# Optimization experiments

Hardware: AMD Instinct MI355X
Metric: run time of the kernel (lower is better)

The kernel has to match this reference:

```python
import math
import jax, jax.numpy as jnp
import numpy as np

B, Q, HID = 4, 4, 4096
NH, NKV, HD = 32, 8, 128
GROUPS = NH // NKV
CACHE_LEN = 4096
CACHE_MAX = CACHE_LEN + 512  # prefill_len + max_len(512)
ROPE_THETA = 500000.0
SCALE = 1.0 / math.sqrt(128.0)  # hardcoded softmax_scale in module


def rotate_half(x):
    x1, x2 = jnp.split(x, 2, axis=-1)
    return jnp.concatenate([-x2, x1], axis=-1)


def setup_inputs() -> dict:
    key = jax.random.key(0)
    ks = jax.random.split(key, 8)
    std = 0.02
    # RoPE angles for positions [CACHE_LEN, CACHE_LEN+Q)
    pos = (CACHE_LEN + jnp.arange(Q)).astype(jnp.float32)
    inv_freq = 1.0 / (ROPE_THETA ** (jnp.arange(0, HD, 2, dtype=jnp.float32) / HD))
    freqs = pos[:, None] * inv_freq[None, :]            # [Q, HD/2]
    emb = jnp.concatenate([freqs, freqs], axis=-1)      # [Q, HD]
    cos = jnp.broadcast_to(jnp.cos(emb)[None], (B, Q, HD)).astype(jnp.float32)
    sin = jnp.broadcast_to(jnp.sin(emb)[None], (B, Q, HD)).astype(jnp.float32)
    return {
        "hidden_states": jax.random.normal(ks[0], (B, Q, HID), jnp.float32),
        "cos": cos,
        "sin": sin,
        "K_Cache": jax.random.normal(ks[1], (B, NKV, CACHE_MAX, HD), jnp.float32) * 0.5,
        "V_Cache": jax.random.normal(ks[2], (B, NKV, CACHE_MAX, HD), jnp.float32) * 0.5,
        "Wq": jax.random.normal(ks[3], (NH * HD, HID), jnp.float32) * std,
        "Wk": jax.random.normal(ks[4], (NKV * HD, HID), jnp.float32) * std,
        "Wv": jax.random.normal(ks[5], (NKV * HD, HID), jnp.float32) * std,
        "Wo": jax.random.normal(ks[6], (HID, NH * HD), jnp.float32) * std,
        "cache_lens": int(CACHE_LEN),
    }


def reference(hidden_states, cos, sin, K_Cache, V_Cache, Wq, Wk, Wv, Wo, cache_lens):
    b, q, _ = hidden_states.shape
    # projections (torch Linear: x @ W.T), reshape to [b, h, q, d]
    qs = jnp.einsum('bsh,oh->bso', hidden_states, Wq).reshape(b, q, NH, HD).transpose(0, 2, 1, 3)
    ks = jnp.einsum('bsh,oh->bso', hidden_states, Wk).reshape(b, q, NKV, HD).transpose(0, 2, 1, 3)
    vs = jnp.einsum('bsh,oh->bso', hidden_states, Wv).reshape(b, q, NKV, HD).transpose(0, 2, 1, 3)
    # RoPE, unsqueeze_dim=1 (head axis)
    c, s = cos[:, None, :, :], sin[:, None, :, :]
    qs = qs * c + rotate_half(qs) * s
    ks = ks * c + rotate_half(ks) * s
    # scatter new K/V into the cache at offset cache_lens
    K_Cache = K_Cache.at[:, :, cache_lens:cache_lens + q, :].set(ks)
    V_Cache = V_Cache.at[:, :, cache_lens:cache_lens + q, :].set(vs)
    # K_total/V_total = cache prefix ++ fresh keys/values; GQA repeat
    K_total = jnp.repeat(jnp.concatenate([K_Cache[:, :, :cache_lens, :], ks], axis=2), GROUPS, axis=1)
    V_total = jnp.repeat(jnp.concatenate([V_Cache[:, :, :cache_lens, :], vs], axis=2), GROUPS, axis=1)
    scores = jnp.einsum('bhqd,bhkd->bhqk', qs, K_total) * SCALE
    # causal mask over the appended q tokens, cache prefix fully visible
    tri = jnp.triu(jnp.ones((q, q), bool), 1)
    mask = jnp.concatenate([jnp.zeros((q, cache_lens), bool), tri], axis=1)
    scores = jnp.where(mask[None, None], -jnp.inf, scores)
    attn = jax.nn.softmax(scores.astype(jnp.float32), axis=-1).astype(V_total.dtype)
    out = jnp.einsum('bhqk,bhkd->bhqd', attn, V_total)
    out = out.transpose(0, 2, 1, 3).reshape(b, q, NH * HD)
    return jnp.einsum('bsh,oh->bso', out, Wo)
```

## Files before the change

kernel.cpp:

```cpp
#include <hip/hip_runtime.h>
#include <math.h>

#define HIDK 4096
#define NHQ 32
#define NKV 8
#define HD 128
#define NROW 16
#define CMAX 4608
#define CLEN 4096
#define NCHUNK 16
#define CHUNK 256
#define SCALE 0.08838834764831845f

__device__ __forceinline__ float4 ld4(const float* p) { return *reinterpret_cast<const float4*>(p); }

__global__ __launch_bounds__(64) void gemm16_kernel(
    const float* __restrict__ X,
    const float* __restrict__ W1, const float* __restrict__ W2, const float* __restrict__ W3,
    int n1, int n2,
    float* __restrict__ o1, int os1,
    float* __restrict__ o2, int os2,
    float* __restrict__ o3, int os3)
{
  const int lane = threadIdx.x;
  const int o = blockIdx.x * 4;

  const float* Wb; float* ob; int os;
  if (o < n1)           { Wb = W1 + (size_t)o * HIDK;            ob = o1 + o;            os = os1; }
  else if (o < n1 + n2) { const int f = o - n1;      Wb = W2 + (size_t)f * HIDK; ob = o2 + f; os = os2; }
  else                  { const int f = o - n1 - n2; Wb = W3 + (size_t)f * HIDK; ob = o3 + f; os = os3; }

  float acc[NROW][4];
  #pragma unroll
  for (int bs = 0; bs < NROW; ++bs)
    #pragma unroll
    for (int r = 0; r < 4; ++r) acc[bs][r] = 0.f;

  for (int i = 0; i < 16; ++i) {
    const int k0 = i * 256 + lane * 4;
    const float4 w0 = ld4(Wb + 0 * HIDK + k0);
    const float4 w1 = ld4(Wb + 1 * HIDK + k0);
    const float4 w2 = ld4(Wb + 2 * HIDK + k0);
    const float4 w3 = ld4(Wb + 3 * HIDK + k0);
    #pragma unroll
    for (int bs = 0; bs < NROW; ++bs) {
      const float4 h = ld4(X + (size_t)bs * HIDK + k0);
      acc[bs][0] += h.x * w0.x + h.y * w0.y + h.z * w0.z + h.w * w0.w;
      acc[bs][1] += h.x * w1.x + h.y * w1.y + h.z * w1.z + h.w * w1.w;
      acc[bs][2] += h.x * w2.x + h.y * w2.y + h.z * w2.z + h.w * w2.w;
      acc[bs][3] += h.x * w3.x + h.y * w3.y + h.z * w3.z + h.w * w3.w;
    }
  }

  #pragma unroll
  for (int m = 1; m < 64; m <<= 1)
    #pragma unroll
    for (int bs = 0; bs < NROW; ++bs)
      #pragma unroll
      for (int r = 0; r < 4; ++r)
        acc[bs][r] += __shfl_xor(acc[bs][r], m, 64);

  if (lane == 0) {
    #pragma unroll
    for (int bs = 0; bs < NROW; ++bs)
      #pragma unroll
      for (int r = 0; r < 4; ++r)
        ob[(size_t)bs * os + r] = acc[bs][r];
  }
}

__global__ __launch_bounds__(512) void attn_chunk_kernel(
    const float* __restrict__ qraw, const float* __restrict__ Kc, const float* __restrict__ Vc,
    const float* __restrict__ cosp, const float* __restrict__ sinp,
    float* __restrict__ partO, float* __restrict__ partM, float* __restrict__ partL)
{
  __shared__ float qsh[16][128];
  __shared__ float P[CHUNK][20];

  const int tid  = threadIdx.x;
  const int lane = tid & 63;
  const int w    = tid >> 6;
  const int bkv   = blockIdx.x >> 4;
  const int chunk = blockIdx.x & 15;
  const int b  = bkv >> 3, kv = bkv & 7;
  const int p0 = chunk * CHUNK;

  for (int e = tid; e < 2048; e += 512) {
    const int r = e >> 7, d = e & 127;
    const int g = r >> 2, s = r & 3;
    const int h = kv * 4 + g;
    const float* qp = qraw + (size_t)(b * 4 + s) * HIDK + h * HD;
    const float c  = cosp[(b * 4 + s) * HD + d];
    const float sn = sinp[(b * 4 + s) * HD + d];
    const float q0 = qp[d], q1 = qp[d ^ 64];
    const float sgn = (d < 64) ? -1.f : 1.f;
    qsh[r][d] = (q0 * c + sgn * q1 * sn) * SCALE;
  }
  __syncthreads();

  {
    const int h2 = w >> 2, pq = w & 3;
    const int dsub = lane & 15, psub = lane >> 4;
    float4 qa[8], qb[8];
    #pragma unroll
    for (int rr = 0; rr < 8; ++rr) {
      qa[rr] = *(const float4*)&qsh[h2 * 8 + rr][dsub * 8];
      qb[rr] = *(const float4*)&qsh[h2 * 8 + rr][dsub * 8 + 4];
    }
    const float* Kbase = Kc + ((size_t)(b * 8 + kv) * CMAX + p0 + pq * 64) * HD;
    #pragma unroll 2
    for (int i = 0; i < 16; ++i) {
      const int pl = i * 4 + psub;
      const float* kp = Kbase + (size_t)pl * HD + dsub * 8;
      const float4 ka = ld4(kp), kb = ld4(kp + 4);
      float sc[8];
      #pragma unroll
      for (int rr = 0; rr < 8; ++rr) {
        sc[rr] = ka.x * qa[rr].x + ka.y * qa[rr].y + ka.z * qa[rr].z + ka.w * qa[rr].w
               + kb.x * qb[rr].x + kb.y * qb[rr].y + kb.z * qb[rr].z + kb.w * qb[rr].w;
      }
      #pragma unroll
      for (int m = 1; m <= 8; m <<= 1)
        #pragma unroll
        for (int rr = 0; rr < 8; ++rr)
          sc[rr] += __shfl_xor(sc[rr], m, 64);
      if (dsub == 0) {
        const int pch = pq * 64 + pl;
        *(float4*)&P[pch][h2 * 8]     = make_float4(sc[0], sc[1], sc[2], sc[3]);
        *(float4*)&P[pch][h2 * 8 + 4] = make_float4(sc[4], sc[5], sc[6], sc[7]);
      }
    }
  }
  __syncthreads();

  {
    #pragma unroll
    for (int rr = 0; rr < 2; ++rr) {
      const int r = w * 2 + rr;
      float v[4];
      #pragma unroll
      for (int k = 0; k < 4; ++k) v[k] = P[lane + 64 * k][r];
      float m = fmaxf(fmaxf(v[0], v[1]), fmaxf(v[2], v[3]));
      #pragma unroll
      for (int mm = 1; mm < 64; mm <<= 1) m = fmaxf(m, __shfl_xor(m, mm, 64));
      float l = 0.f;
      #pragma unroll
      for (int k = 0; k < 4; ++k) { v[k] = __expf(v[k] - m); l += v[k]; }
      #pragma unroll
      for (int mm = 1; mm < 64; mm <<= 1) l += __shfl_xor(l, mm, 64);
      #pragma unroll
      for (int k = 0; k < 4; ++k) P[lane + 64 * k][r] = v[k];
      if (lane == 0) {
        const int g = r >> 2, s = r & 3, h = kv * 4 + g;
        const int idx = ((b * NHQ + h) * 4 + s) * NCHUNK + chunk;
        partM[idx] = m;
        partL[idx] = l;
      }
    }
  }
  __syncthreads();

  {
    const int h2 = w >> 2, dq = w & 3;
    const int dl = lane & 31, ph = lane >> 5;
    float o[8];
    #pragma unroll
    for (int rr = 0; rr < 8; ++rr) o[rr] = 0.f;
    const float* Vbase = Vc + ((size_t)(b * 8 + kv) * CMAX + p0 + ph * 128) * HD + dq * 32 + dl;
    #pragma unroll 4
    for (int p = 0; p < 128; ++p) {
      const float vv = Vbase[(size_t)p * HD];
      const int pch = ph * 128 + p;
      const float4 pa = *(const float4*)&P[pch][h2 * 8];
      const float4 pb = *(const float4*)&P[pch][h2 * 8 + 4];
      o[0] += pa.x * vv; o[1] += pa.y * vv; o[2] += pa.z * vv; o[3] += pa.w * vv;
      o[4] += pb.x * vv; o[5] += pb.y * vv; o[6] += pb.z * vv; o[7] += pb.w * vv;
    }
    #pragma unroll
    for (int rr = 0; rr < 8; ++rr) o[rr] += __shfl_xor(o[rr], 32, 64);
    if (ph == 0) {
      const int d = dq * 32 + dl;
      #pragma unroll
      for (int rr = 0; rr < 8; ++rr) {
        const int r = h2 * 8 + rr;
        const int g = r >> 2, s = r & 3, h = kv * 4 + g;
        const size_t idx = ((size_t)((b * NHQ + h) * 4 + s) * NCHUNK + chunk) * HD + d;
        partO[idx] = o[rr];
      }
    }
  }
}

__global__ __launch_bounds__(64) void combine_kernel(
    const float* __restrict__ qraw, const float* __restrict__ kraw, const float* __restrict__ vraw,
    const float* __restrict__ cosp, const float* __restrict__ sinp,
    const float* __restrict__ partO, const float* __restrict__ partM, const float* __restrict__ partL,
    float* __restrict__ attn)
{
  const int bid = blockIdx.x;
  const int s = bid & 3;
  const int h = (bid >> 2) & 31;
  const int b = bid >> 7;
  const int kv = h >> 2;
  const int lane = threadIdx.x;
  const int d0 = lane * 2;

  float mc[NCHUNK], lc[NCHUNK];
  float M = -INFINITY;
  #pragma unroll
  for (int c = 0; c < NCHUNK; ++c) {
    mc[c] = partM[bid * NCHUNK + c];
    lc[c] = partL[bid * NCHUNK + c];
    M = fmaxf(M, mc[c]);
  }

  float qr0, qr1;
  {
    const float* qp = qraw + (size_t)(b * 4 + s) * HIDK + h * HD;
    const float c0 = cosp[(b * 4 + s) * HD + d0],     sn0 = sinp[(b * 4 + s) * HD + d0];
    const float c1 = cosp[(b * 4 + s) * HD + d0 + 1], sn1 = sinp[(b * 4 + s) * HD + d0 + 1];
    const float sg0 = (d0 < 64) ? -1.f : 1.f;
    const float sg1 = ((d0 + 1) < 64) ? -1.f : 1.f;
    qr0 = (qp[d0] * c0 + sg0 * qp[d0 ^ 64] * sn0) * SCALE;
    qr1 = (qp[d0 + 1] * c1 + sg1 * qp[(d0 + 1) ^ 64] * sn1) * SCALE;
  }

  float sj[4] = {0.f, 0.f, 0.f, 0.f};
  float Mp = M;
  #pragma unroll
  for (int j = 0; j < 4; ++j) {
    if (j <= s) {
      const float* kp = kraw + (size_t)(b * 4 + j) * 1024 + kv * HD;
      const float c0 = cosp[(b * 4 + j) * HD + d0],     sn0 = sinp[(b * 4 + j) * HD + d0];
      const float c1 = cosp[(b * 4 + j) * HD + d0 + 1], sn1 = sinp[(b * 4 + j) * HD + d0 + 1];
      const float sg0 = (d0 < 64) ? -1.f : 1.f;
      const float sg1 = ((d0 + 1) < 64) ? -1.f : 1.f;
      const float kr0 = kp[d0] * c0 + sg0 * kp[d0 ^ 64] * sn0;
      const float kr1 = kp[d0 + 1] * c1 + sg1 * kp[(d0 + 1) ^ 64] * sn1;
      float part = qr0 * kr0 + qr1 * kr1;
      #pragma unroll
      for (int m = 1; m < 64; m <<= 1) part += __shfl_xor(part, m, 64);
      sj[j] = part;
      Mp = fmaxf(Mp, part);
    }
  }

  float ltot = 0.f;
  float O0 = 0.f, O1 = 0.f;
  #pragma unroll
  for (int c = 0; c < NCHUNK; ++c) {
    const float a = __expf(mc[c] - Mp);
    ltot += lc[c] * a;
    const float2 v = *(const float2*)&partO[((size_t)bid * NCHUNK + c) * HD + d0];
    O0 += a * v.x;
    O1 += a * v.y;
  }
  #pragma unroll
  for (int j = 0; j < 4; ++j) {
    if (j <= s) {
      const float e = __expf(sj[j] - Mp);
      ltot += e;
      const float* vp = vraw + (size_t)(b * 4 + j) * 1024 + kv * HD + d0;
      O0 += e * vp[0];
      O1 += e * vp[1];
    }
  }
  const float inv = 1.f / ltot;
  *(float2*)&attn[(size_t)(b * 4 + s) * HIDK + h * HD + d0] = make_float2(O0 * inv, O1 * inv);
}

extern "C" void kernel_launch(void* const* d_in, const int* in_sizes, int n_in,
                              void* d_out, int out_size, void* d_ws, size_t ws_size,
                              hipStream_t stream)
{
  const float* hid  = (const float*)d_in[0];
  const float* cosp = (const float*)d_in[1];
  const float* sinp = (const float*)d_in[2];
  const float* Kc   = (const float*)d_in[3];
  const float* Vc   = (const float*)d_in[4];
  const float* Wq   = (const float*)d_in[5];
  const float* Wk   = (const float*)d_in[6];
  const float* Wv   = (const float*)d_in[7];
  const float* Wo   = (const float*)d_in[8];
  float* out = (float*)d_out;

  float* ws    = (float*)d_ws;
  float* qraw  = ws;
  float* kraw  = ws + 65536;
  float* vraw  = ws + 81920;
  float* attn  = ws + 98304;
  float* partO = ws + 163840;
  float* partM = ws + 1212416;
  float* partL = ws + 1220608;

  gemm16_kernel<<<1536, 64, 0, stream>>>(hid, Wq, Wk, Wv, 4096, 1024,
                                         qraw, 4096, kraw, 1024, vraw, 1024);
  attn_chunk_kernel<<<512, 512, 0, stream>>>(qraw, Kc, Vc, cosp, sinp, partO, partM, partL);
  combine_kernel<<<512, 64, 0, stream>>>(qraw, kraw, vraw, cosp, sinp, partO, partM, partL, attn);
  gemm16_kernel<<<1024, 64, 0, stream>>>(attn, Wo, Wo, Wo, 4096, 0,
                                         out, 4096, out, 4096, out, 4096);
}
```

Baseline: 129.6 us.

## Split attention blocks by head pair and chunk, restructure GEMV to one row per wave

Measured after the change: 328.5 us. 2.53x slower.

```diff
diff --git a/kernel.cpp b/kernel.cpp
--- a/kernel.cpp
+++ b/kernel.cpp
@@ -3,18 +3,15 @@
 
 #define HIDK 4096
 #define NHQ 32
-#define NKV 8
 #define HD 128
-#define NROW 16
 #define CMAX 4608
 #define CLEN 4096
-#define NCHUNK 16
-#define CHUNK 256
 #define SCALE 0.08838834764831845f
 
 __device__ __forceinline__ float4 ld4(const float* p) { return *reinterpret_cast<const float4*>(p); }
-
-__global__ __launch_bounds__(64) void gemm16_kernel(
+__device__ __forceinline__ float dot4(float4 a, float4 b) { return a.x*b.x + a.y*b.y + a.z*b.z + a.w*b.w; }
+
+__global__ __launch_bounds__(256, 6) void gemm1_kernel(
     const float* __restrict__ X,
     const float* __restrict__ W1, const float* __restrict__ W2, const float* __restrict__ W3,
     int n1, int n2,
@@ -22,175 +19,160 @@
     float* __restrict__ o2, int os2,
     float* __restrict__ o3, int os3)
 {
-  const int lane = threadIdx.x;
-  const int o = blockIdx.x * 4;
+  const int lane = threadIdx.x & 63;
+  const int o = blockIdx.x * 4 + (threadIdx.x >> 6);
 
   const float* Wb; float* ob; int os;
   if (o < n1)           { Wb = W1 + (size_t)o * HIDK;            ob = o1 + o;            os = os1; }
   else if (o < n1 + n2) { const int f = o - n1;      Wb = W2 + (size_t)f * HIDK; ob = o2 + f; os = os2; }
   else                  { const int f = o - n1 - n2; Wb = W3 + (size_t)f * HIDK; ob = o3 + f; os = os3; }
 
-  float acc[NROW][4];
-  #pragma unroll
-  for (int bs = 0; bs < NROW; ++bs)
-    #pragma unroll
-    for (int r = 0; r < 4; ++r) acc[bs][r] = 0.f;
-
-  for (int i = 0; i < 16; ++i) {
-    const int k0 = i * 256 + lane * 4;
-    const float4 w0 = ld4(Wb + 0 * HIDK + k0);
-    const float4 w1 = ld4(Wb + 1 * HIDK + k0);
-    const float4 w2 = ld4(Wb + 2 * HIDK + k0);
-    const float4 w3 = ld4(Wb + 3 * HIDK + k0);
-    #pragma unroll
-    for (int bs = 0; bs < NROW; ++bs) {
-      const float4 h = ld4(X + (size_t)bs * HIDK + k0);
-      acc[bs][0] += h.x * w0.x + h.y * w0.y + h.z * w0.z + h.w * w0.w;
-      acc[bs][1] += h.x * w1.x + h.y * w1.y + h.z * w1.z + h.w * w1.w;
-      acc[bs][2] += h.x * w2.x + h.y * w2.y + h.z * w2.z + h.w * w2.w;
-      acc[bs][3] += h.x * w3.x + h.y * w3.y + h.z * w3.z + h.w * w3.w;
+  float acc[16];
+  #pragma unroll
+  for (int b = 0; b < 16; ++b) acc[b] = 0.f;
+
+  #pragma unroll
+  for (int h = 0; h < 2; ++h) {
+    float4 w[8];
+    #pragma unroll
+    for (int i = 0; i < 8; ++i) w[i] = ld4(Wb + h * 2048 + i * 256 + lane * 4);
+    #pragma unroll
+    for (int i = 0; i < 8; ++i) {
+      const int k0 = h * 2048 + i * 256 + lane * 4;
+      #pragma unroll
+      for (int b = 0; b < 16; ++b)
+        acc[b] += dot4(ld4(X + (size_t)b * HIDK + k0), w[i]);
     }
   }
 
   #pragma unroll
   for (int m = 1; m < 64; m <<= 1)
     #pragma unroll
-    for (int bs = 0; bs < NROW; ++bs)
-      #pragma unroll
-      for (int r = 0; r < 4; ++r)
-        acc[bs][r] += __shfl_xor(acc[bs][r], m, 64);
+    for (int b = 0; b < 16; ++b) acc[b] += __shfl_xor(acc[b], m, 64);
 
   if (lane == 0) {
     #pragma unroll
-    for (int bs = 0; bs < NROW; ++bs)
-      #pragma unroll
-      for (int r = 0; r < 4; ++r)
-        ob[(size_t)bs * os + r] = acc[bs][r];
-  }
-}
-
-__global__ __launch_bounds__(512) void attn_chunk_kernel(
+    for (int b = 0; b < 16; ++b) ob[(size_t)b * os] = acc[b];
+  }
+}
+
+template <int CH>
+__global__ __launch_bounds__(256, 6) void attn_kernel(
     const float* __restrict__ qraw, const float* __restrict__ Kc, const float* __restrict__ Vc,
     const float* __restrict__ cosp, const float* __restrict__ sinp,
     float* __restrict__ partO, float* __restrict__ partM, float* __restrict__ partL)
 {
-  __shared__ float qsh[16][128];
-  __shared__ float P[CHUNK][20];
-
-  const int tid  = threadIdx.x;
-  const int lane = tid & 63;
-  const int w    = tid >> 6;
-  const int bkv   = blockIdx.x >> 4;
-  const int chunk = blockIdx.x & 15;
-  const int b  = bkv >> 3, kv = bkv & 7;
-  const int p0 = chunk * CHUNK;
-
-  for (int e = tid; e < 2048; e += 512) {
+  constexpr int NCH = CLEN / CH;
+  __shared__ float qsh[8][128];
+  __shared__ float P[CH][12];
+
+  const int tid = threadIdx.x, lane = tid & 63, w = tid >> 6;
+  const int chunk = blockIdx.x % NCH;
+  const int bh = blockIdx.x / NCH;
+  const int hp = bh & 1;
+  const int bkv = bh >> 1;
+  const int b = bkv >> 3, kv = bkv & 7;
+  const int p0 = chunk * CH;
+  const int h0 = kv * 4 + hp * 2;
+
+  #pragma unroll
+  for (int e = tid; e < 1024; e += 256) {
     const int r = e >> 7, d = e & 127;
-    const int g = r >> 2, s = r & 3;
-    const int h = kv * 4 + g;
+    const int hl = r >> 2, s = r & 3;
+    const int h = h0 + hl;
     const float* qp = qraw + (size_t)(b * 4 + s) * HIDK + h * HD;
     const float c  = cosp[(b * 4 + s) * HD + d];
     const float sn = sinp[(b * 4 + s) * HD + d];
-    const float q0 = qp[d], q1 = qp[d ^ 64];
     const float sgn = (d < 64) ? -1.f : 1.f;
-    qsh[r][d] = (q0 * c + sgn * q1 * sn) * SCALE;
+    qsh[r][d] = (qp[d] * c + sgn * qp[d ^ 64] * sn) * SCALE;
   }
   __syncthreads();
 
   {
-    const int h2 = w >> 2, pq = w & 3;
-    const int dsub = lane & 15, psub = lane >> 4;
-    float4 qa[8], qb[8];
-    #pragma unroll
-    for (int rr = 0; rr < 8; ++rr) {
-      qa[rr] = *(const float4*)&qsh[h2 * 8 + rr][dsub * 8];
-      qb[rr] = *(const float4*)&qsh[h2 * 8 + rr][dsub * 8 + 4];
-    }
-    const float* Kbase = Kc + ((size_t)(b * 8 + kv) * CMAX + p0 + pq * 64) * HD;
+    const int dsub = lane & 31, psub = lane >> 5;
+    float4 q[8];
+    #pragma unroll
+    for (int r = 0; r < 8; ++r) q[r] = ld4(&qsh[r][dsub * 4]);
+    constexpr int PPW = CH / 4;
+    const float* Kbase = Kc + ((size_t)(b * 8 + kv) * CMAX + p0 + w * PPW) * HD + dsub * 4;
     #pragma unroll 2
-    for (int i = 0; i < 16; ++i) {
-      const int pl = i * 4 + psub;
-      const float* kp = Kbase + (size_t)pl * HD + dsub * 8;
-      const float4 ka = ld4(kp), kb = ld4(kp + 4);
+    for (int i = 0; i < PPW / 2; ++i) {
+      const int pl = i * 2 + psub;
+      const float4 k4 = ld4(Kbase + (size_t)pl * HD);
       float sc[8];
       #pragma unroll
-      for (int rr = 0; rr < 8; ++rr) {
-        sc[rr] = ka.x * qa[rr].x + ka.y * qa[rr].y + ka.z * qa[rr].z + ka.w * qa[rr].w
-               + kb.x * qb[rr].x + kb.y * qb[rr].y + kb.z * qb[rr].z + kb.w * qb[rr].w;
+      for (int r = 0; r < 8; ++r) sc[r] = dot4(k4, q[r]);
+      #pragma unroll
+      for (int m = 1; m < 32; m <<= 1)
+        #pragma unroll
+        for (int r = 0; r < 8; ++r) sc[r] += __shfl_xor(sc[r], m, 64);
+      if (dsub == 0) {
+        *(float4*)&P[w * PPW + pl][0] = make_float4(sc[0], sc[1], sc[2], sc[3]);
+        *(float4*)&P[w * PPW + pl][4] = make_float4(sc[4], sc[5], sc[6], sc[7]);
       }
-      #pragma unroll
-      for (int m = 1; m <= 8; m <<= 1)
-        #pragma unroll
-        for (int rr = 0; rr < 8; ++rr)
-          sc[rr] += __shfl_xor(sc[rr], m, 64);
-      if (dsub == 0) {
-        const int pch = pq * 64 + pl;
-        *(float4*)&P[pch][h2 * 8]     = make_float4(sc[0], sc[1], sc[2], sc[3]);
-        *(float4*)&P[pch][h2 * 8 + 4] = make_float4(sc[4], sc[5], sc[6], sc[7]);
-      }
     }
   }
   __syncthreads();
 
   {
+    constexpr int NPL = CH / 64;
     #pragma unroll
     for (int rr = 0; rr < 2; ++rr) {
       const int r = w * 2 + rr;
-      float v[4];
-      #pragma unroll
-      for (int k = 0; k < 4; ++k) v[k] = P[lane + 64 * k][r];
-      float m = fmaxf(fmaxf(v[0], v[1]), fmaxf(v[2], v[3]));
-      #pragma unroll
-      for (int mm = 1; mm < 64; mm <<= 1) m = fmaxf(m, __shfl_xor(m, mm, 64));
+      float v[NPL];
+      float mx = -INFINITY;
+      #pragma unroll
+      for (int k = 0; k < NPL; ++k) { v[k] = P[lane + 64 * k][r]; mx = fmaxf(mx, v[k]); }
+      #pragma unroll
+      for (int m = 1; m < 64; m <<= 1) mx = fmaxf(mx, __shfl_xor(mx, m, 64));
       float l = 0.f;
       #pragma unroll
-      for (int k = 0; k < 4; ++k) { v[k] = __expf(v[k] - m); l += v[k]; }
-      #pragma unroll
-      for (int mm = 1; mm < 64; mm <<= 1) l += __shfl_xor(l, mm, 64);
-      #pragma unroll
-      for (int k = 0; k < 4; ++k) P[lane + 64 * k][r] = v[k];
+      for (int k = 0; k < NPL; ++k) { v[k] = __expf(v[k] - mx); l += v[k]; }
+      #pragma unroll
+      for (int m = 1; m < 64; m <<= 1) l += __shfl_xor(l, m, 64);
+      #pragma unroll
+      for (int k = 0; k < NPL; ++k) P[lane + 64 * k][r] = v[k];
       if (lane == 0) {
-        const int g = r >> 2, s = r & 3, h = kv * 4 + g;
-        const int idx = ((b * NHQ + h) * 4 + s) * NCHUNK + chunk;
-        partM[idx] = m;
-        partL[idx] = l;
+        const int hl = r >> 2, s = r & 3, h = h0 + hl;
+        const int row = (b * NHQ + h) * 4 + s;
+        partM[row * NCH + chunk] = mx;
+        partL[row * NCH + chunk] = l;
       }
     }
   }
   __syncthreads();
 
   {
-    const int h2 = w >> 2, dq = w & 3;
     const int dl = lane & 31, ph = lane >> 5;
+    const int d = w * 32 + dl;
     float o[8];
     #pragma unroll
-    for (int rr = 0; rr < 8; ++rr) o[rr] = 0.f;
-    const float* Vbase = Vc + ((size_t)(b * 8 + kv) * CMAX + p0 + ph * 128) * HD + dq * 32 + dl;
+    for (int r = 0; r < 8; ++r) o[r] = 0.f;
+    constexpr int HP = CH / 2;
+    const float* Vbase = Vc + ((size_t)(b * 8 + kv) * CMAX + p0 + ph * HP) * HD + d;
     #pragma unroll 4
-    for (int p = 0; p < 128; ++p) {
+    for (int p = 0; p < HP; ++p) {
       const float vv = Vbase[(size_t)p * HD];
-      const int pch = ph * 128 + p;
-      const float4 pa = *(const float4*)&P[pch][h2 * 8];
-      const float4 pb = *(const float4*)&P[pch][h2 * 8 + 4];
+      const int pc = ph * HP + p;
+      const float4 pa = *(const float4*)&P[pc][0];
+      const float4 pb = *(const float4*)&P[pc][4];
       o[0] += pa.x * vv; o[1] += pa.y * vv; o[2] += pa.z * vv; o[3] += pa.w * vv;
       o[4] += pb.x * vv; o[5] += pb.y * vv; o[6] += pb.z * vv; o[7] += pb.w * vv;
     }
     #pragma unroll
-    for (int rr = 0; rr < 8; ++rr) o[rr] += __shfl_xor(o[rr], 32, 64);
+    for (int r = 0; r < 8; ++r) o[r] += __shfl_xor(o[r], 32, 64);
     if (ph == 0) {
-      const int d = dq * 32 + dl;
-      #pragma unroll
-      for (int rr = 0; rr < 8; ++rr) {
-        const int r = h2 * 8 + rr;
-        const int g = r >> 2, s = r & 3, h = kv * 4 + g;
-        const size_t idx = ((size_t)((b * NHQ + h) * 4 + s) * NCHUNK + chunk) * HD + d;
-        partO[idx] = o[rr];
+      #pragma unroll
+      for (int r = 0; r < 8; ++r) {
+        const int hl = r >> 2, s = r & 3, h = h0 + hl;
+        const size_t row = (size_t)(b * NHQ + h) * 4 + s;
+        partO[(row * NCH + chunk) * HD + d] = o[r];
       }
     }
   }
 }
 
+template <int NCH>
 __global__ __launch_bounds__(64) void combine_kernel(
     const float* __restrict__ qraw, const float* __restrict__ kraw, const float* __restrict__ vraw,
     const float* __restrict__ cosp, const float* __restrict__ sinp,
@@ -205,12 +187,12 @@
   const int lane = threadIdx.x;
   const int d0 = lane * 2;
 
-  float mc[NCHUNK], lc[NCHUNK];
+  float mc[NCH], lc[NCH];
   float M = -INFINITY;
   #pragma unroll
-  for (int c = 0; c < NCHUNK; ++c) {
-    mc[c] = partM[bid * NCHUNK + c];
-    lc[c] = partL[bid * NCHUNK + c];
+  for (int c = 0; c < NCH; ++c) {
+    mc[c] = partM[bid * NCH + c];
+    lc[c] = partL[bid * NCH + c];
     M = fmaxf(M, mc[c]);
   }
 
@@ -245,15 +227,17 @@
     }
   }
 
-  float ltot = 0.f;
-  float O0 = 0.f, O1 = 0.f;
-  #pragma unroll
-  for (int c = 0; c < NCHUNK; ++c) {
-    const float a = __expf(mc[c] - Mp);
-    ltot += lc[c] * a;
-    const float2 v = *(const float2*)&partO[((size_t)bid * NCHUNK + c) * HD + d0];
-    O0 += a * v.x;
-    O1 += a * v.y;
+  float a[NCH];
+  #pragma unroll
+  for (int c = 0; c < NCH; ++c) a[c] = __expf(mc[c] - Mp);
+
+  float ltot = 0.f, O0 = 0.f, O1 = 0.f;
+  #pragma unroll 4
+  for (int c = 0; c < NCH; ++c) {
+    ltot += lc[c] * a[c];
+    const float2 v = *(const float2*)&partO[((size_t)bid * NCH + c) * HD + d0];
+    O0 += a[c] * v.x;
+    O1 += a[c] * v.y;
   }
   #pragma unroll
   for (int j = 0; j < 4; ++j) {
@@ -290,13 +274,21 @@
   float* vraw  = ws + 81920;
   float* attn  = ws + 98304;
   float* partO = ws + 163840;
-  float* partM = ws + 1212416;
-  float* partL = ws + 1220608;
-
-  gemm16_kernel<<<1536, 64, 0, stream>>>(hid, Wq, Wk, Wv, 4096, 1024,
+  const bool big = ws_size >= (size_t)2293760 * sizeof(float);
+  const int nch = big ? 32 : 16;
+  float* partM = partO + (size_t)512 * nch * 128;
+  float* partL = partM + (size_t)512 * nch;
+
+  gemm1_kernel<<<1536, 256, 0, stream>>>(hid, Wq, Wk, Wv, 4096, 1024,
                                          qraw, 4096, kraw, 1024, vraw, 1024);
-  attn_chunk_kernel<<<512, 512, 0, stream>>>(qraw, Kc, Vc, cosp, sinp, partO, partM, partL);
-  combine_kernel<<<512, 64, 0, stream>>>(qraw, kraw, vraw, cosp, sinp, partO, partM, partL, attn);
-  gemm16_kernel<<<1024, 64, 0, stream>>>(attn, Wo, Wo, Wo, 4096, 0,
+  if (big)
+    attn_kernel<128><<<64 * 32, 256, 0, stream>>>(qraw, Kc, Vc, cosp, sinp, partO, partM, partL);
+  else
+    attn_kernel<256><<<64 * 16, 256, 0, stream>>>(qraw, Kc, Vc, cosp, sinp, partO, partM, partL);
+  if (big)
+    combine_kernel<32><<<512, 64, 0, stream>>>(qraw, kraw, vraw, cosp, sinp, partO, partM, partL, attn);
+  else
+    combine_kernel<16><<<512, 64, 0, stream>>>(qraw, kraw, vraw, cosp, sinp, partO, partM, partL, attn);
+  gemm1_kernel<<<1024, 256, 0, stream>>>(attn, Wo, Wo, Wo, 4096, 0,
                                          out, 4096, out, 4096, out, 4096);
 }
```
